# Kernel tuning notes

Measured on AMD Instinct MI355X. Metric: run time of the kernel, lower is better.

The kernel has to match this reference:

```python
import jax, jax.numpy as jnp
import numpy as np

B, S, D, H = 64, 197, 1024, 4096

# I-BERT IntGELU constants: erf(x) ~ a*(x+b)^2 + c on [0,-b], integer-only form
K_SQRT2 = 1.4142          # sqrt(2)
GELU_SHIFT = 14           # 2**14 right-shift to avoid accumulator overflow
COEF_A = -0.2888
COEF_B = -1.769
COEF_C = 1.0 / COEF_A     # c folded by a, as in I-BERT (coeff[2] /= coeff[0])


def setup_inputs() -> dict:
    key = jax.random.key(0)
    k1, k2, k3, k4, k5, k6 = jax.random.split(key, 6)
    x_int = jax.random.randint(k1, (B, S, D), 0, 127).astype(jnp.int32)  # int8-range activations
    s_x = jax.random.uniform(k2, (1,), jnp.float32, 0.01, 0.03)          # per-tensor act scale
    w1 = jax.random.normal(k3, (H, D), jnp.float32) * 0.02
    b1 = jax.random.normal(k4, (H,), jnp.float32) * 0.02
    w2 = jax.random.normal(k5, (D, H), jnp.float32) * 0.02
    b2 = jax.random.normal(k6, (D,), jnp.float32) * 0.02
    return {"x_int": x_int, "s_x": s_x, "w1": w1, "b1": b1, "w2": w2, "b2": b2}


def _quant_weight(w):
    # per-tensor symmetric int8 weight quantization (QuantLinearWithWeight)
    s_w = jnp.max(jnp.abs(w)) / 127.0
    w_int = jnp.clip(jnp.round(w / s_w), -127.0, 127.0)
    return w_int, s_w


def _quant_linear(x_int, s_x, w, b):
    # integer GEMM: int8 acts x int8 weights -> int32 accumulator, scale s_x*s_w
    w_int, s_w = _quant_weight(w)
    s_out = s_x * s_w
    b_int = jnp.round(b / s_out)  # bias quantized into the accumulator scale
    acc = jnp.einsum('bsd,hd->bsh', x_int, w_int) + b_int
    return acc, s_out


def _int_erf(x_int, sf):
    # integer polynomial approx of erf (I-BERT)
    b_int = jnp.floor(COEF_B / sf)
    c_int = jnp.floor(COEF_C / sf ** 2)
    sign = jnp.sign(x_int)
    abs_int = jnp.minimum(jnp.abs(x_int), -b_int)
    y_int = sign * ((abs_int + b_int) ** 2 + c_int)
    sf_out = sf ** 2 * COEF_A
    y_int = jnp.floor(y_int / 2.0 ** GELU_SHIFT)  # shift to keep accumulator in range
    return y_int, sf_out * 2.0 ** GELU_SHIFT


def _int_gelu(x_int, sf):
    # GELU(x) = x * 0.5 * (1 + erf(x/sqrt(2))), integer-only
    sig_int, sig_sf = _int_erf(x_int, sf / K_SQRT2)
    shift_int = jnp.floor(1.0 / sig_sf)  # torch: 1.0 // sigmoid_scaling_factor
    y_int = x_int * (sig_int + shift_int)
    return y_int, sf * sig_sf / 2.0


def _quant_act(x_int, sf):
    # QuantAct: requantize int32-scale activations back to int8 (dynamic per-tensor scale)
    x_hat = x_int * sf
    s_a = jnp.max(jnp.abs(x_hat)) / 127.0
    q = jnp.clip(jnp.round(x_hat / s_a), -128.0, 127.0)
    return q, s_a


def reference(x_int, s_x, w1, b1, w2, b2):
    x = x_int.astype(jnp.float32)
    s = s_x[0]
    x, s = _quant_linear(x, s, w1, b1)   # [B,S,H] int32 accumulator
    x, s = _int_gelu(x, s)               # integer-only GELU
    x, s = _quant_act(x, s)              # requant -> int8 range
    # dropout_1 is identity in eval mode
    x, s = _quant_linear(x, s, w2, b2)   # [B,S,D] int32 accumulator
    # dropout_2 is identity in eval mode
    return x, s
```

## Files before the change

### kernel.cpp

```cpp
#include <hip/hip_runtime.h>
#include <cstdint>
#include <cstddef>

constexpr int Bb = 64, Ss = 197, Dd = 1024, Hh = 4096;
constexpr int M  = Bb * Ss;
constexpr int MT = (M + 127) / 128;
constexpr int Mpad = MT * 128;
constexpr int NBLK1 = (Hh / 128) * MT;

#define SL_S1    4
#define SL_BERF  5
#define SL_CERF  6
#define SL_SHIFT 7
#define SL_S2    8
#define SL_SA    9
#define SL_SOUT2 10
#define SL_SW1   11
#define SL_SW2   12

typedef int v4i __attribute__((ext_vector_type(4)));

#define GLD_LDS(g, l) \
  __builtin_amdgcn_global_load_lds((const __attribute__((address_space(1))) void*)(g), \
                                   (__attribute__((address_space(3))) void*)(l), 16, 0, 0)

__device__ __forceinline__ float blockmax256(float m) {
  #pragma unroll
  for (int off = 32; off; off >>= 1) m = fmaxf(m, __shfl_down(m, off, 64));
  __shared__ float wm[4];
  int lane = threadIdx.x & 63, wid = threadIdx.x >> 6;
  if (lane == 0) wm[wid] = m;
  __syncthreads();
  return fmaxf(fmaxf(wm[0], wm[1]), fmaxf(wm[2], wm[3]));
}

__global__ void k_wmax(const float* __restrict__ w1, const float* __restrict__ w2,
                       int n4, float* __restrict__ pmax) {
  int b = blockIdx.x;
  const float4* s4 = (const float4*)(b < 512 ? w1 : w2);
  float m = 0.f;
  for (int i = (b & 511) * 256 + threadIdx.x; i < n4; i += 512 * 256) {
    float4 v = s4[i];
    m = fmaxf(m, fmaxf(fmaxf(fabsf(v.x), fabsf(v.y)), fmaxf(fabsf(v.z), fabsf(v.w))));
  }
  m = blockmax256(m);
  if (threadIdx.x == 0) pmax[b] = m;
}

__global__ void k_scalars1(unsigned* slu, const float* __restrict__ pmax,
                           const float* __restrict__ s_x_ptr) {
  int t = threadIdx.x;
  float m1 = fmaxf(pmax[t], pmax[t + 256]);
  float m2 = fmaxf(pmax[512 + t], pmax[768 + t]);
  __shared__ float r1[256], r2[256];
  r1[t] = m1; r2[t] = m2;
  __syncthreads();
  for (int s = 128; s; s >>= 1) {
    if (t < s) { r1[t] = fmaxf(r1[t], r1[t + s]); r2[t] = fmaxf(r2[t], r2[t + s]); }
    __syncthreads();
  }
  if (t == 0) {
    float* slf = (float*)slu;
    float s_w1 = r1[0] / 127.0f;
    float s_w2 = r2[0] / 127.0f;
    float s1  = s_x_ptr[0] * s_w1;
    float sfe = s1 / 1.4142f;
    float berf = floorf(-1.769f / sfe);
    float cerf = floorf(((float)(1.0 / -0.2888)) / (sfe * sfe));
    float sig  = ((sfe * sfe) * -0.2888f) * 16384.0f;
    float shiftv = floorf(1.0f / sig);
    float s2 = (s1 * sig) / 2.0f;
    slf[SL_S1] = s1; slf[SL_BERF] = berf; slf[SL_CERF] = cerf;
    slf[SL_SHIFT] = shiftv; slf[SL_S2] = s2; slf[SL_SW1] = s_w1; slf[SL_SW2] = s_w2;
  }
}

__global__ void k_scalars2(unsigned* slu, const float* __restrict__ pmax,
                           float* dout_scalar) {
  int t = threadIdx.x;
  float m = 0.f;
  for (int i = t; i < NBLK1; i += 256) m = fmaxf(m, pmax[i]);
  __shared__ float r1[256];
  r1[t] = m;
  __syncthreads();
  for (int s = 128; s; s >>= 1) {
    if (t < s) r1[t] = fmaxf(r1[t], r1[t + s]);
    __syncthreads();
  }
  if (t == 0) {
    float* slf = (float*)slu;
    float xm = fabsf(r1[0] * slf[SL_S2]);
    float sa = xm / 127.0f;
    float sout2 = sa * slf[SL_SW2];
    slf[SL_SA] = sa; slf[SL_SOUT2] = sout2;
    *dout_scalar = sout2;
  }
}

__global__ void k_quantcvt(const float* __restrict__ w1, const float* __restrict__ w2,
                           const int* __restrict__ x, const unsigned* __restrict__ slu,
                           int8_t* __restrict__ w1q, int8_t* __restrict__ w2q,
                           int8_t* __restrict__ xq) {
  const float* slf = (const float*)slu;
  float sw1 = slf[SL_SW1], sw2 = slf[SL_SW2];
  const int n1 = Hh * Dd / 4, n2 = Dd * Hh / 4;
  const int nx = M * Dd / 4, n3 = Mpad * Dd / 4;
  const int total = n1 + n2 + n3;
  for (int i = blockIdx.x * blockDim.x + threadIdx.x; i < total; i += gridDim.x * blockDim.x) {
    if (i < n1 + n2) {
      bool first = i < n1;
      int idx = first ? i : i - n1;
      float sw = first ? sw1 : sw2;
      float4 v = ((const float4*)(first ? w1 : w2))[idx];
      int qa = (int)fminf(fmaxf(rintf(v.x / sw), -127.f), 127.f);
      int qb = (int)fminf(fmaxf(rintf(v.y / sw), -127.f), 127.f);
      int qc = (int)fminf(fmaxf(rintf(v.z / sw), -127.f), 127.f);
      int qd = (int)fminf(fmaxf(rintf(v.w / sw), -127.f), 127.f);
      unsigned p = (unsigned)(qa & 0xff) | ((unsigned)(qb & 0xff) << 8) |
                   ((unsigned)(qc & 0xff) << 16) | ((unsigned)(qd & 0xff) << 24);
      ((unsigned*)(first ? w1q : w2q))[idx] = p;
    } else {
      int idx = i - n1 - n2;
      unsigned p = 0u;
      if (idx < nx) {
        int4 v = ((const int4*)x)[idx];
        p = (unsigned)(v.x & 0xff) | ((unsigned)(v.y & 0xff) << 8) |
            ((unsigned)(v.z & 0xff) << 16) | ((unsigned)(v.w & 0xff) << 24);
      }
      ((unsigned*)xq)[idx] = p;
    }
  }
}

template <int K, int MODE>
__global__ __launch_bounds__(256) void k_gemm(
    const int8_t* __restrict__ A, const int8_t* __restrict__ Bm,
    const float* __restrict__ bias, const unsigned* __restrict__ slu,
    int8_t* __restrict__ qout, float* __restrict__ fout, float* __restrict__ pmax_y,
    int Mreal, int Ncols) {
  __shared__ alignas(16) int8_t smem[32768];
  int8_t* As = smem;
  int8_t* Bs = smem + 16384;
  const int t = threadIdx.x;
  const int bm = blockIdx.y, bn = blockIdx.x;
  const int lane = t & 63, wid = t >> 6;
  const int wRow = (wid >> 1) * 64, wCol = (wid & 1) * 64;
  const int lm = lane & 15, quad = lane >> 4;

  v4i acc[4][4] = {};

  const size_t aBase = (size_t)bm * 128 * K;
  const size_t bBase = (size_t)bn * 128 * K;

  for (int k0 = 0; k0 < K; k0 += 128) {
    #pragma unroll
    for (int c = 0; c < 4; c++) {
      int s = c * 256 + t;
      int row = s >> 3;
      int cb = (s & 7) ^ (row & 7);
      size_t goff = (size_t)row * K + k0 + cb * 16;
      GLD_LDS(A + aBase + goff, As + s * 16);
      GLD_LDS(Bm + bBase + goff, Bs + s * 16);
    }
    __syncthreads();
    #pragma unroll
    for (int ks = 0; ks < 2; ks++) {
      v4i af[4], bf[4];
      #pragma unroll
      for (int i = 0; i < 4; i++) {
        int r = wRow + i * 16 + lm;
        af[i] = *(const v4i*)(As + r * 128 + (((ks * 4 + quad) ^ (r & 7)) << 4));
      }
      #pragma unroll
      for (int i = 0; i < 4; i++) {
        int r = wCol + i * 16 + lm;
        bf[i] = *(const v4i*)(Bs + r * 128 + (((ks * 4 + quad) ^ (r & 7)) << 4));
      }
      #pragma unroll
      for (int i = 0; i < 4; i++)
        #pragma unroll
        for (int j = 0; j < 4; j++)
          acc[i][j] = __builtin_amdgcn_mfma_i32_16x16x64_i8(bf[j], af[i], acc[i][j], 0, 0, 0);
    }
    __syncthreads();
  }

  const float* slf = (const float*)slu;
  if constexpr (MODE == 2) {
    float sout2 = slf[SL_SOUT2];
    float4 bq[4];
    #pragma unroll
    for (int j = 0; j < 4; j++) {
      float4 bv = *(const float4*)(bias + bn * 128 + wCol + j * 16 + quad * 4);
      bq[j].x = rintf(bv.x / sout2); bq[j].y = rintf(bv.y / sout2);
      bq[j].z = rintf(bv.z / sout2); bq[j].w = rintf(bv.w / sout2);
    }
    #pragma unroll
    for (int i = 0; i < 4; i++) {
      int gr = bm * 128 + wRow + i * 16 + lm;
      if (gr < Mreal) {
        #pragma unroll
        for (int j = 0; j < 4; j++) {
          int gc0 = bn * 128 + wCol + j * 16 + quad * 4;
          float4 o;
          o.x = (float)acc[i][j][0] + bq[j].x;
          o.y = (float)acc[i][j][1] + bq[j].y;
          o.z = (float)acc[i][j][2] + bq[j].z;
          o.w = (float)acc[i][j][3] + bq[j].w;
          *(float4*)(fout + (size_t)gr * Ncols + gc0) = o;
        }
      }
    }
  } else {
    float s1 = slf[SL_S1], berf = slf[SL_BERF], cerf = slf[SL_CERF], shiftv = slf[SL_SHIFT];
    float s2 = slf[SL_S2];
    float sa = (MODE == 1) ? slf[SL_SA] : 1.0f;
    float r_req = (MODE == 1) ? (s2 / sa) : 1.0f;
    float lmax = 0.f;
    float4 bq[4];
    #pragma unroll
    for (int j = 0; j < 4; j++) {
      float4 bv = *(const float4*)(bias + bn * 128 + wCol + j * 16 + quad * 4);
      bq[j].x = rintf(bv.x / s1); bq[j].y = rintf(bv.y / s1);
      bq[j].z = rintf(bv.z / s1); bq[j].w = rintf(bv.w / s1);
    }
    #pragma unroll
    for (int i = 0; i < 4; i++) {
      int mrow = wRow + i * 16 + lm;
      int gr = bm * 128 + mrow;
      bool rowok = gr < Mreal;
      #pragma unroll
      for (int j = 0; j < 4; j++) {
        int n0 = wCol + j * 16 + quad * 4;
        unsigned packed = 0u;
        #pragma unroll
        for (int r = 0; r < 4; r++) {
          float a = (float)acc[i][j][r] + ((const float*)&bq[j])[r];
          float ax = fminf(fabsf(a), -berf);
          float tt = ax + berf;
          float u = tt * tt + cerf;
          float ye = (a < 0.f) ? -u : u;
          float yv = floorf(ye * (1.0f / 16384.0f));
          float y = a * (yv + shiftv);
          if constexpr (MODE == 0) {
            if (rowok) lmax = fmaxf(lmax, fabsf(y));
          } else {
            float qf = rintf(y * r_req);
            qf = fminf(fmaxf(qf, -128.f), 127.f);
            packed |= ((unsigned)((int)qf & 0xff)) << (8 * r);
          }
        }
        if constexpr (MODE == 1) {
          *(unsigned*)(smem + mrow * 132 + n0) = packed;
        }
      }
    }
    if constexpr (MODE == 0) {
      #pragma unroll
      for (int off = 32; off; off >>= 1) lmax = fmaxf(lmax, __shfl_down(lmax, off, 64));
      float* red = (float*)smem;
      if (lane == 0) red[wid] = lmax;
      __syncthreads();
      if (t == 0) {
        float b = fmaxf(fmaxf(red[0], red[1]), fmaxf(red[2], red[3]));
        pmax_y[bm * gridDim.x + bn] = b;
      }
    } else {
      __syncthreads();
      #pragma unroll
      for (int c2 = 0; c2 < 4; c2++) {
        int idx = c2 * 256 + t;
        int row = idx >> 3, c16 = (idx & 7) << 4;
        v4i v = *(const v4i*)(smem + row * 132 + c16);
        *(v4i*)(qout + (size_t)(bm * 128 + row) * Ncols + bn * 128 + c16) = v;
      }
    }
  }
}

extern "C" void kernel_launch(void* const* d_in, const int* in_sizes, int n_in,
                              void* d_out, int out_size, void* d_ws, size_t ws_size,
                              hipStream_t stream) {
  const int*   x   = (const int*)d_in[0];
  const float* s_x = (const float*)d_in[1];
  const float* w1  = (const float*)d_in[2];
  const float* b1  = (const float*)d_in[3];
  const float* w2  = (const float*)d_in[4];
  const float* b2  = (const float*)d_in[5];
  float* out = (float*)d_out;

  char* ws = (char*)d_ws;
  unsigned* slots = (unsigned*)ws;
  float* pmax_w = (float*)(ws + 1024);
  float* pmax_y = (float*)(ws + 8192);
  int8_t* w1q = (int8_t*)(ws + 32768);
  int8_t* w2q = w1q + (size_t)Hh * Dd;
  int8_t* xq  = w2q + (size_t)Dd * Hh;
  int8_t* qbuf = xq + (size_t)Mpad * Dd;

  k_wmax<<<1024, 256, 0, stream>>>(w1, w2, Hh * Dd / 4, pmax_w);
  k_scalars1<<<1, 256, 0, stream>>>(slots, pmax_w, s_x);
  k_quantcvt<<<1024, 256, 0, stream>>>(w1, w2, x, slots, w1q, w2q, xq);

  dim3 g1(Hh / 128, MT);
  k_gemm<Dd, 0><<<g1, 256, 0, stream>>>(xq, w1q, b1, slots, nullptr, nullptr,
                                        pmax_y, M, Hh);
  k_scalars2<<<1, 256, 0, stream>>>(slots, pmax_y, out + (size_t)M * Dd);
  k_gemm<Dd, 1><<<g1, 256, 0, stream>>>(xq, w1q, b1, slots, qbuf, nullptr,
                                        nullptr, M, Hh);
  dim3 g2(Dd / 128, MT);
  k_gemm<Hh, 2><<<g2, 256, 0, stream>>>(qbuf, w2q, b2, slots, nullptr, out,
                                        nullptr, M, Dd);
}
```

Baseline: 397.0 us.

## Compute first GEMM once, store fp32 GELU output, requantize in separate pass

Replaces the two-pass recompute of the first GEMM (one pass for the global max, one for quantization) with a single GEMM that writes fp32 GELU results and per-block maxima. A separate elementwise kernel then requantizes the buffer to int8. This removes a full redundant int8 GEMM but adds a large fp32 write and read of the intermediate activation. The new path runs only when the workspace is big enough.

```diff
diff --git a/kernel.cpp b/kernel.cpp
--- a/kernel.cpp
+++ b/kernel.cpp
@@ -132,6 +132,29 @@
   }
 }
 
+__global__ __launch_bounds__(256) void k_requant(const float* __restrict__ y,
+                                                 const unsigned* __restrict__ slu,
+                                                 int8_t* __restrict__ q) {
+  const float* slf = (const float*)slu;
+  float r_req = slf[SL_S2] / slf[SL_SA];
+  const int n16 = M * Hh / 16;
+  for (int i = blockIdx.x * blockDim.x + threadIdx.x; i < n16; i += gridDim.x * blockDim.x) {
+    const float4* yp = (const float4*)y + (size_t)i * 4;
+    unsigned pk[4];
+    #pragma unroll
+    for (int v = 0; v < 4; v++) {
+      float4 t = yp[v];
+      int a = (int)fminf(fmaxf(rintf(t.x * r_req), -128.f), 127.f);
+      int b = (int)fminf(fmaxf(rintf(t.y * r_req), -128.f), 127.f);
+      int c = (int)fminf(fmaxf(rintf(t.z * r_req), -128.f), 127.f);
+      int d = (int)fminf(fmaxf(rintf(t.w * r_req), -128.f), 127.f);
+      pk[v] = (unsigned)(a & 0xff) | ((unsigned)(b & 0xff) << 8) |
+              ((unsigned)(c & 0xff) << 16) | ((unsigned)(d & 0xff) << 24);
+    }
+    *(v4i*)(q + (size_t)i * 16) = *(const v4i*)pk;
+  }
+}
+
 template <int K, int MODE>
 __global__ __launch_bounds__(256) void k_gemm(
     const int8_t* __restrict__ A, const int8_t* __restrict__ Bm,
@@ -233,6 +256,7 @@
       for (int j = 0; j < 4; j++) {
         int n0 = wCol + j * 16 + quad * 4;
         unsigned packed = 0u;
+        float4 y4;
         #pragma unroll
         for (int r = 0; r < 4; r++) {
           float a = (float)acc[i][j][r] + ((const float*)&bq[j])[r];
@@ -244,6 +268,9 @@
           float y = a * (yv + shiftv);
           if constexpr (MODE == 0) {
             if (rowok) lmax = fmaxf(lmax, fabsf(y));
+          } else if constexpr (MODE == 3) {
+            if (rowok) lmax = fmaxf(lmax, fabsf(y));
+            ((float*)&y4)[r] = y;
           } else {
             float qf = rintf(y * r_req);
             qf = fminf(fmaxf(qf, -128.f), 127.f);
@@ -253,9 +280,12 @@
         if constexpr (MODE == 1) {
           *(unsigned*)(smem + mrow * 132 + n0) = packed;
         }
-      }
-    }
-    if constexpr (MODE == 0) {
+        if constexpr (MODE == 3) {
+          if (rowok) *(float4*)(fout + (size_t)gr * Ncols + bn * 128 + n0) = y4;
+        }
+      }
+    }
+    if constexpr (MODE == 0 || MODE == 3) {
       #pragma unroll
       for (int off = 32; off; off >>= 1) lmax = fmaxf(lmax, __shfl_down(lmax, off, 64));
       float* red = (float*)smem;
@@ -297,17 +327,28 @@
   int8_t* w2q = w1q + (size_t)Hh * Dd;
   int8_t* xq  = w2q + (size_t)Dd * Hh;
   int8_t* qbuf = xq + (size_t)Mpad * Dd;
+  float*  ybuf = (float*)(qbuf + (size_t)Mpad * Hh);
+
+  size_t need = 32768 + 2 * (size_t)Hh * Dd + (size_t)Mpad * Dd
+              + (size_t)Mpad * Hh + (size_t)M * Hh * 4;
 
   k_wmax<<<1024, 256, 0, stream>>>(w1, w2, Hh * Dd / 4, pmax_w);
   k_scalars1<<<1, 256, 0, stream>>>(slots, pmax_w, s_x);
   k_quantcvt<<<1024, 256, 0, stream>>>(w1, w2, x, slots, w1q, w2q, xq);
 
   dim3 g1(Hh / 128, MT);
-  k_gemm<Dd, 0><<<g1, 256, 0, stream>>>(xq, w1q, b1, slots, nullptr, nullptr,
-                                        pmax_y, M, Hh);
-  k_scalars2<<<1, 256, 0, stream>>>(slots, pmax_y, out + (size_t)M * Dd);
-  k_gemm<Dd, 1><<<g1, 256, 0, stream>>>(xq, w1q, b1, slots, qbuf, nullptr,
-                                        nullptr, M, Hh);
+  if (ws_size >= need) {
+    k_gemm<Dd, 3><<<g1, 256, 0, stream>>>(xq, w1q, b1, slots, nullptr, ybuf,
+                                          pmax_y, M, Hh);
+    k_scalars2<<<1, 256, 0, stream>>>(slots, pmax_y, out + (size_t)M * Dd);
+    k_requant<<<2048, 256, 0, stream>>>(ybuf, slots, qbuf);
+  } else {
+    k_gemm<Dd, 0><<<g1, 256, 0, stream>>>(xq, w1q, b1, slots, nullptr, nullptr,
+                                          pmax_y, M, Hh);
+    k_scalars2<<<1, 256, 0, stream>>>(slots, pmax_y, out + (size_t)M * Dd);
+    k_gemm<Dd, 1><<<g1, 256, 0, stream>>>(xq, w1q, b1, slots, qbuf, nullptr,
+                                          nullptr, M, Hh);
+  }
   dim3 g2(Dd / 128, MT);
   k_gemm<Hh, 2><<<g2, 256, 0, stream>>>(qbuf, w2q, b2, slots, nullptr, out,
                                         nullptr, M, Dd);
```

New measurement: 383.4 us. 1.04x faster.

## Use 256x256 double-buffered int8 GEMM tiles with 8-wave ping-pong scheduling

Applied to the files above, without the earlier changes.

Replaces the 128x128 single-buffered GEMM with 256x256 tiles on 512 threads. LDS is double-buffered at 128KB, and the next k-tile's global-to-LDS loads are interleaved with MFMA phases using explicit barriers, vmcnt waits and setprio. The aim is to hide load latency and raise operand reuse per block. In exchange, fewer blocks launch: the second GEMM gets only 200 blocks, which may leave CUs idle. LDS use now limits occupancy to one block per CU.

```diff
diff --git a/kernel.cpp b/kernel.cpp
--- a/kernel.cpp
+++ b/kernel.cpp
@@ -4,9 +4,9 @@
 
 constexpr int Bb = 64, Ss = 197, Dd = 1024, Hh = 4096;
 constexpr int M  = Bb * Ss;
-constexpr int MT = (M + 127) / 128;
-constexpr int Mpad = MT * 128;
-constexpr int NBLK1 = (Hh / 128) * MT;
+constexpr int MT = (M + 255) / 256;
+constexpr int Mpad = MT * 256;
+constexpr int NBLK1 = (Hh / 256) * MT;
 
 #define SL_S1    4
 #define SL_BERF  5
@@ -23,6 +23,9 @@
 #define GLD_LDS(g, l) \
   __builtin_amdgcn_global_load_lds((const __attribute__((address_space(1))) void*)(g), \
                                    (__attribute__((address_space(3))) void*)(l), 16, 0, 0)
+
+#define PBAR() asm volatile("s_barrier" ::: "memory")
+#define SCHED_FENCE() __builtin_amdgcn_sched_barrier(0)
 
 __device__ __forceinline__ float blockmax256(float m) {
   #pragma unroll
@@ -133,56 +136,127 @@
 }
 
 template <int K, int MODE>
-__global__ __launch_bounds__(256) void k_gemm(
+__global__ __launch_bounds__(512, 2) void k_gemm(
     const int8_t* __restrict__ A, const int8_t* __restrict__ Bm,
     const float* __restrict__ bias, const unsigned* __restrict__ slu,
     int8_t* __restrict__ qout, float* __restrict__ fout, float* __restrict__ pmax_y,
     int Mreal, int Ncols) {
-  __shared__ alignas(16) int8_t smem[32768];
-  int8_t* As = smem;
-  int8_t* Bs = smem + 16384;
+  constexpr int NK = K / 128;
+  __shared__ alignas(64) int8_t smem[131072];
   const int t = threadIdx.x;
   const int bm = blockIdx.y, bn = blockIdx.x;
   const int lane = t & 63, wid = t >> 6;
-  const int wRow = (wid >> 1) * 64, wCol = (wid & 1) * 64;
+  const int wr = wid >> 2, wc = wid & 3;
   const int lm = lane & 15, quad = lane >> 4;
 
-  v4i acc[4][4] = {};
-
-  const size_t aBase = (size_t)bm * 128 * K;
-  const size_t bBase = (size_t)bn * 128 * K;
-
-  for (int k0 = 0; k0 < K; k0 += 128) {
-    #pragma unroll
-    for (int c = 0; c < 4; c++) {
-      int s = c * 256 + t;
-      int row = s >> 3;
-      int cb = (s & 7) ^ (row & 7);
-      size_t goff = (size_t)row * K + k0 + cb * 16;
-      GLD_LDS(A + aBase + goff, As + s * 16);
-      GLD_LDS(Bm + bBase + goff, Bs + s * 16);
-    }
-    __syncthreads();
-    #pragma unroll
-    for (int ks = 0; ks < 2; ks++) {
-      v4i af[4], bf[4];
-      #pragma unroll
-      for (int i = 0; i < 4; i++) {
-        int r = wRow + i * 16 + lm;
-        af[i] = *(const v4i*)(As + r * 128 + (((ks * 4 + quad) ^ (r & 7)) << 4));
-      }
-      #pragma unroll
-      for (int i = 0; i < 4; i++) {
-        int r = wCol + i * 16 + lm;
-        bf[i] = *(const v4i*)(Bs + r * 128 + (((ks * 4 + quad) ^ (r & 7)) << 4));
-      }
-      #pragma unroll
-      for (int i = 0; i < 4; i++)
-        #pragma unroll
-        for (int j = 0; j < 4; j++)
-          acc[i][j] = __builtin_amdgcn_mfma_i32_16x16x64_i8(bf[j], af[i], acc[i][j], 0, 0, 0);
-    }
-    __syncthreads();
+  const int srow = t >> 2;
+  const int scc  = (t & 3) ^ ((srow >> 1) & 3);
+  const int8_t* aSrc = A  + (size_t)(bm * 256 + srow) * K + scc * 16;
+  const int8_t* bSrc = Bm + (size_t)(bn * 256 + srow) * K + scc * 16;
+
+  int aoff[8], boff[4];
+  #pragma unroll
+  for (int i = 0; i < 8; i++) {
+    int r = wr * 128 + i * 16 + lm;
+    aoff[i] = r * 64 + ((quad ^ ((r >> 1) & 3)) << 4);
+  }
+  #pragma unroll
+  for (int j = 0; j < 4; j++) {
+    int r = wc * 64 + j * 16 + lm;
+    boff[j] = r * 64 + ((quad ^ ((r >> 1) & 3)) << 4);
+  }
+
+  v4i acc[8][4] = {};
+
+  auto stA = [&](int buf, int kt, int ks) {
+    int8_t* d = smem + buf * 65536 + ks * 16384 + t * 16;
+    const int8_t* s = aSrc + kt * 128 + ks * 64;
+    GLD_LDS(s, d);
+    GLD_LDS(s + (size_t)128 * K, d + 8192);
+  };
+  auto stB = [&](int buf, int kt, int ks) {
+    int8_t* d = smem + buf * 65536 + 32768 + ks * 16384 + t * 16;
+    const int8_t* s = bSrc + kt * 128 + ks * 64;
+    GLD_LDS(s, d);
+    GLD_LDS(s + (size_t)128 * K, d + 8192);
+  };
+
+  stB(0, 0, 0); stA(0, 0, 0); stB(0, 0, 1); stA(0, 0, 1);
+  asm volatile("s_waitcnt vmcnt(4)" ::: "memory");
+  SCHED_FENCE();
+  PBAR();
+
+  #pragma unroll 1
+  for (int kt = 0; kt < NK; ++kt) {
+    const int cb = kt & 1, nb = cb ^ 1;
+    const int8_t* Ac = smem + cb * 65536;
+    const int8_t* Bc = Ac + 32768;
+    const bool pf = (kt + 1 < NK);
+    v4i bf[4], af[4];
+
+    #pragma unroll
+    for (int j = 0; j < 4; j++) bf[j] = *(const v4i*)(Bc + boff[j]);
+    #pragma unroll
+    for (int i = 0; i < 4; i++) af[i] = *(const v4i*)(Ac + aoff[i]);
+    if (pf) stB(nb, kt + 1, 0);
+    PBAR();
+    __builtin_amdgcn_s_setprio(1);
+    #pragma unroll
+    for (int i = 0; i < 4; i++)
+      #pragma unroll
+      for (int j = 0; j < 4; j++)
+        acc[i][j] = __builtin_amdgcn_mfma_i32_16x16x64_i8(bf[j], af[i], acc[i][j], 0, 0, 0);
+    __builtin_amdgcn_s_setprio(0);
+    SCHED_FENCE();
+    PBAR();
+
+    #pragma unroll
+    for (int i = 0; i < 4; i++) af[i] = *(const v4i*)(Ac + aoff[4 + i]);
+    if (pf) stA(nb, kt + 1, 0);
+    PBAR();
+    __builtin_amdgcn_s_setprio(1);
+    #pragma unroll
+    for (int i = 0; i < 4; i++)
+      #pragma unroll
+      for (int j = 0; j < 4; j++)
+        acc[4 + i][j] = __builtin_amdgcn_mfma_i32_16x16x64_i8(bf[j], af[i], acc[4 + i][j], 0, 0, 0);
+    __builtin_amdgcn_s_setprio(0);
+    if (pf) asm volatile("s_waitcnt vmcnt(4)" ::: "memory");
+    else    asm volatile("s_waitcnt vmcnt(0)" ::: "memory");
+    SCHED_FENCE();
+    PBAR();
+
+    #pragma unroll
+    for (int j = 0; j < 4; j++) bf[j] = *(const v4i*)(Bc + 16384 + boff[j]);
+    #pragma unroll
+    for (int i = 0; i < 4; i++) af[i] = *(const v4i*)(Ac + 16384 + aoff[i]);
+    if (pf) stB(nb, kt + 1, 1);
+    PBAR();
+    __builtin_amdgcn_s_setprio(1);
+    #pragma unroll
+    for (int i = 0; i < 4; i++)
+      #pragma unroll
+      for (int j = 0; j < 4; j++)
+        acc[i][j] = __builtin_amdgcn_mfma_i32_16x16x64_i8(bf[j], af[i], acc[i][j], 0, 0, 0);
+    __builtin_amdgcn_s_setprio(0);
+    SCHED_FENCE();
+    PBAR();
+
+    #pragma unroll
+    for (int i = 0; i < 4; i++) af[i] = *(const v4i*)(Ac + 16384 + aoff[4 + i]);
+    if (pf) stA(nb, kt + 1, 1);
+    PBAR();
+    __builtin_amdgcn_s_setprio(1);
+    #pragma unroll
+    for (int i = 0; i < 4; i++)
+      #pragma unroll
+      for (int j = 0; j < 4; j++)
+        acc[4 + i][j] = __builtin_amdgcn_mfma_i32_16x16x64_i8(bf[j], af[i], acc[4 + i][j], 0, 0, 0);
+    __builtin_amdgcn_s_setprio(0);
+    if (pf) asm volatile("s_waitcnt vmcnt(4)" ::: "memory");
+    else    asm volatile("s_waitcnt vmcnt(0)" ::: "memory");
+    SCHED_FENCE();
+    PBAR();
   }
 
   const float* slf = (const float*)slu;
@@ -191,17 +265,17 @@
     float4 bq[4];
     #pragma unroll
     for (int j = 0; j < 4; j++) {
-      float4 bv = *(const float4*)(bias + bn * 128 + wCol + j * 16 + quad * 4);
+      float4 bv = *(const float4*)(bias + bn * 256 + wc * 64 + j * 16 + quad * 4);
       bq[j].x = rintf(bv.x / sout2); bq[j].y = rintf(bv.y / sout2);
       bq[j].z = rintf(bv.z / sout2); bq[j].w = rintf(bv.w / sout2);
     }
     #pragma unroll
-    for (int i = 0; i < 4; i++) {
-      int gr = bm * 128 + wRow + i * 16 + lm;
+    for (int i = 0; i < 8; i++) {
+      int gr = bm * 256 + wr * 128 + i * 16 + lm;
       if (gr < Mreal) {
         #pragma unroll
         for (int j = 0; j < 4; j++) {
-          int gc0 = bn * 128 + wCol + j * 16 + quad * 4;
+          int gc0 = bn * 256 + wc * 64 + j * 16 + quad * 4;
           float4 o;
           o.x = (float)acc[i][j][0] + bq[j].x;
           o.y = (float)acc[i][j][1] + bq[j].y;
@@ -220,18 +294,18 @@
     float4 bq[4];
     #pragma unroll
     for (int j = 0; j < 4; j++) {
-      float4 bv = *(const float4*)(bias + bn * 128 + wCol + j * 16 + quad * 4);
+      float4 bv = *(const float4*)(bias + bn * 256 + wc * 64 + j * 16 + quad * 4);
       bq[j].x = rintf(bv.x / s1); bq[j].y = rintf(bv.y / s1);
       bq[j].z = rintf(bv.z / s1); bq[j].w = rintf(bv.w / s1);
     }
     #pragma unroll
-    for (int i = 0; i < 4; i++) {
-      int mrow = wRow + i * 16 + lm;
-      int gr = bm * 128 + mrow;
+    for (int i = 0; i < 8; i++) {
+      int mrow = wr * 128 + i * 16 + lm;
+      int gr = bm * 256 + mrow;
       bool rowok = gr < Mreal;
       #pragma unroll
       for (int j = 0; j < 4; j++) {
-        int n0 = wCol + j * 16 + quad * 4;
+        int n0 = wc * 64 + j * 16 + quad * 4;
         unsigned packed = 0u;
         #pragma unroll
         for (int r = 0; r < 4; r++) {
@@ -251,7 +325,7 @@
           }
         }
         if constexpr (MODE == 1) {
-          *(unsigned*)(smem + mrow * 132 + n0) = packed;
+          *(unsigned*)(smem + mrow * 272 + n0) = packed;
         }
       }
     }
@@ -262,17 +336,18 @@
       if (lane == 0) red[wid] = lmax;
       __syncthreads();
       if (t == 0) {
-        float b = fmaxf(fmaxf(red[0], red[1]), fmaxf(red[2], red[3]));
+        float b = fmaxf(fmaxf(fmaxf(red[0], red[1]), fmaxf(red[2], red[3])),
+                        fmaxf(fmaxf(red[4], red[5]), fmaxf(red[6], red[7])));
         pmax_y[bm * gridDim.x + bn] = b;
       }
     } else {
       __syncthreads();
       #pragma unroll
-      for (int c2 = 0; c2 < 4; c2++) {
-        int idx = c2 * 256 + t;
-        int row = idx >> 3, c16 = (idx & 7) << 4;
-        v4i v = *(const v4i*)(smem + row * 132 + c16);
-        *(v4i*)(qout + (size_t)(bm * 128 + row) * Ncols + bn * 128 + c16) = v;
+      for (int c2 = 0; c2 < 8; c2++) {
+        int idx = c2 * 512 + t;
+        int row = idx >> 4, c16 = (idx & 15) << 4;
+        v4i v = *(const v4i*)(smem + row * 272 + c16);
+        *(v4i*)(qout + (size_t)(bm * 256 + row) * Ncols + bn * 256 + c16) = v;
       }
     }
   }
@@ -302,13 +377,13 @@
   k_scalars1<<<1, 256, 0, stream>>>(slots, pmax_w, s_x);
   k_quantcvt<<<1024, 256, 0, stream>>>(w1, w2, x, slots, w1q, w2q, xq);
 
-  dim3 g1(Hh / 128, MT);
-  k_gemm<Dd, 0><<<g1, 256, 0, stream>>>(xq, w1q, b1, slots, nullptr, nullptr,
+  dim3 g1(Hh / 256, MT);
+  k_gemm<Dd, 0><<<g1, 512, 0, stream>>>(xq, w1q, b1, slots, nullptr, nullptr,
                                         pmax_y, M, Hh);
   k_scalars2<<<1, 256, 0, stream>>>(slots, pmax_y, out + (size_t)M * Dd);
-  k_gemm<Dd, 1><<<g1, 256, 0, stream>>>(xq, w1q, b1, slots, qbuf, nullptr,
+  k_gemm<Dd, 1><<<g1, 512, 0, stream>>>(xq, w1q, b1, slots, qbuf, nullptr,
                                         nullptr, M, Hh);
-  dim3 g2(Dd / 128, MT);
-  k_gemm<Hh, 2><<<g2, 256, 0, stream>>>(qbuf, w2q, b2, slots, nullptr, out,
+  dim3 g2(Dd / 256, MT);
+  k_gemm<Hh, 2><<<g2, 512, 0, stream>>>(qbuf, w2q, b2, slots, nullptr, out,
                                         nullptr, M, Dd);
 }
```

New measurement: 383.9 us. 3.3% less time.
